# Optimization experiments

Measured on AMD Instinct MI355X. Metric: run time of the kernel, lower is better.

The kernel has to match this reference:

```python
import jax, jax.numpy as jnp
import numpy as np

N_DRUG, N_TARGET, N_EDGES, H = 50000, 20000, 500000, 256


def setup_inputs() -> dict:
    key = jax.random.key(0)
    ks = jax.random.split(key, 6)
    s = 1.0 / np.sqrt(2 * H)
    return {
        "z_drug": jax.random.normal(ks[0], (N_DRUG, H), dtype=jnp.float32),
        "z_target": jax.random.normal(ks[1], (N_TARGET, H), dtype=jnp.float32),
        "row": jax.random.randint(ks[2], (N_EDGES,), 0, N_DRUG, dtype=jnp.int64),
        "col": jax.random.randint(ks[3], (N_EDGES,), 0, N_TARGET, dtype=jnp.int64),
        "W1": jax.random.normal(ks[4], (2 * H, H), dtype=jnp.float32) * s,
        "b1": jnp.zeros((H,), dtype=jnp.float32),
        "W2": jax.random.normal(ks[5], (H, 1), dtype=jnp.float32) * (1.0 / np.sqrt(H)),
        "b2": jnp.zeros((1,), dtype=jnp.float32),
    }


def reference(z_drug, z_target, row, col, W1, b1, W2, b2):
    # gather endpoint embeddings by edge index, concat -> [E, 2H]
    zc = jnp.concatenate([z_drug[row], z_target[col]], axis=-1)
    h = jax.nn.relu(zc @ W1 + b1)          # [E, H]
    return h @ W2 + b2                     # [E, 1]
```

## Files before the change

kernel.cpp:

```cpp
#include <hip/hip_runtime.h>
#include <hip/hip_bf16.h>
#include <stdint.h>


typedef unsigned short u16;
typedef __attribute__((ext_vector_type(8))) short short8;
typedef __attribute__((ext_vector_type(4))) float f32x4;

#define HDIM 256
#define KDIM 512
#define BK 64

__device__ __forceinline__ u16 f2bf(float f) {
  union { float f; uint32_t u; } v; v.f = f;
  uint32_t u = v.u;
  return (u16)((u + 0x7fffu + ((u >> 16) & 1u)) >> 16);
}
__device__ __forceinline__ u16 f2h(float f) {
  union { _Float16 h; u16 u; } v; v.h = (_Float16)f;
  return v.u;
}
__device__ __forceinline__ float h2f(u16 b) {
  union { _Float16 h; u16 u; } v; v.u = b;
  return (float)v.h;
}

__device__ __forceinline__ void gl2lds16(const void* g, void* l) {
  __builtin_amdgcn_global_load_lds(
      (const __attribute__((address_space(1))) unsigned int*)g,
      (__attribute__((address_space(3))) unsigned int*)l,
      16, 0, 0);
}

__global__ void prep_w1t(const float* __restrict__ w1, u16* __restrict__ w1t) {
  const int b = blockIdx.x;
  __shared__ float tile[64][65];
  const int k0 = (b >> 2) * 64, n0 = (b & 3) * 64;
  const int tx = threadIdx.x & 63, ty = threadIdx.x >> 6;
#pragma unroll
  for (int i = ty; i < 64; i += 4)
    tile[i][tx] = w1[(size_t)(k0 + i) * HDIM + n0 + tx];
  __syncthreads();
#pragma unroll
  for (int i = ty; i < 64; i += 4)
    w1t[(size_t)(n0 + i) * KDIM + k0 + tx] = f2bf(tile[tx][i]);
}

__global__ __launch_bounds__(256, 2) void uv_gemm(
    const float* __restrict__ zdf, const float* __restrict__ ztf,
    const u16* __restrict__ w1t, const float* __restrict__ b1,
    u16* __restrict__ Uh, u16* __restrict__ Vh,
    int ND, int NT, int nUb) {
  __shared__ u16 lB[2][128 * BK];

  const int bid = blockIdx.x;
  const int isV = (bid >= nUb);
  const int lb  = isV ? (bid - nUb) : bid;
  const float* zf = isV ? ztf : zdf;
  u16* Oh = isV ? Vh : Uh;
  const int NR = isV ? NT : ND;
  const int r0 = (lb >> 1) * 128;
  const int n0 = (lb & 1) * 128;
  const int kb = isV ? 4 : 0;

  const int tid   = threadIdx.x;
  const int wid   = tid >> 6;
  const int lane  = tid & 63;
  const int r8    = lane >> 3;
  const int slog  = ((lane & 7) ^ (r8 & 7)) * 8;
  const int colid = lane & 15;
  const int quad  = lane >> 4;
  const int csw   = colid & 7;

  const u16* pB = w1t + (uint32_t)(n0 + wid * 32 + r8) * KDIM + slog;
  u16* lBw0 = &lB[0][(wid * 32) * BK];
  u16* lBw1 = &lB[1][(wid * 32) * BK];

  uint32_t offR[2];
#pragma unroll
  for (int rt = 0; rt < 2; ++rt) {
    int r = min(r0 + wid * 32 + rt * 16 + colid, NR - 1);
    offR[rt] = (uint32_t)r * HDIM;
  }

  f32x4 acc[2][8];
#pragma unroll
  for (int i = 0; i < 2; ++i)
#pragma unroll
    for (int j = 0; j < 8; ++j) acc[i][j] = f32x4{0.f, 0.f, 0.f, 0.f};

  float4 a32[2][2][2][2];
  short8 aB[2][2][2];

  auto loadA = [&](int kc, int buf) {
#pragma unroll
    for (int rt = 0; rt < 2; ++rt)
#pragma unroll
      for (int s = 0; s < 2; ++s) {
        const float* p = zf + offR[rt] + kc * BK + s * 32 + quad * 8;
        a32[buf][rt][s][0] = ((const float4*)p)[0];
        a32[buf][rt][s][1] = ((const float4*)p)[1];
      }
  };
  auto cvtA = [&](int buf) {
#pragma unroll
    for (int rt = 0; rt < 2; ++rt)
#pragma unroll
      for (int s = 0; s < 2; ++s) {
        float4 lo = a32[buf][rt][s][0], hi = a32[buf][rt][s][1];
        short8 r;
        r[0] = (short)f2bf(lo.x); r[1] = (short)f2bf(lo.y);
        r[2] = (short)f2bf(lo.z); r[3] = (short)f2bf(lo.w);
        r[4] = (short)f2bf(hi.x); r[5] = (short)f2bf(hi.y);
        r[6] = (short)f2bf(hi.z); r[7] = (short)f2bf(hi.w);
        aB[buf][rt][s] = r;
      }
  };
  auto stageB = [&](int kch, u16* dst) {
#pragma unroll
    for (int t = 0; t < 4; ++t)
      gl2lds16(pB + (size_t)t * 8 * KDIM + kch * BK, dst + t * 8 * BK);
  };

  stageB(kb, lBw0);
  loadA(0, 0);
  asm volatile("s_waitcnt vmcnt(0)" ::: "memory");
  cvtA(0);
  __builtin_amdgcn_s_barrier();

#pragma unroll
  for (int kc = 0; kc < 4; ++kc) {
    const int cur = kc & 1, nxt = cur ^ 1;
    if (kc < 3) {
      stageB(kb + kc + 1, nxt ? lBw1 : lBw0);
      loadA(kc + 1, nxt);
    }
#pragma unroll
    for (int s = 0; s < 2; ++s) {
      const int sl = s * 4 + quad;
      __builtin_amdgcn_s_setprio(1);
#pragma unroll
      for (int ct = 0; ct < 8; ++ct) {
        short8 bF = *(const short8*)
            &lB[cur][(ct * 16 + colid) * BK + ((sl ^ csw) * 8)];
        acc[0][ct] = __builtin_amdgcn_mfma_f32_16x16x32_bf16(
            aB[cur][0][s], bF, acc[0][ct], 0, 0, 0);
        acc[1][ct] = __builtin_amdgcn_mfma_f32_16x16x32_bf16(
            aB[cur][1][s], bF, acc[1][ct], 0, 0, 0);
      }
      __builtin_amdgcn_s_setprio(0);
    }
    if (kc < 3) {
      asm volatile("s_waitcnt vmcnt(0)" ::: "memory");
      cvtA(nxt);
      __builtin_amdgcn_s_barrier();
    }
  }

  float b1v[8];
#pragma unroll
  for (int ct = 0; ct < 8; ++ct)
    b1v[ct] = isV ? 0.f : b1[n0 + ct * 16 + colid];
#pragma unroll
  for (int rt = 0; rt < 2; ++rt)
#pragma unroll
    for (int j = 0; j < 4; ++j) {
      int r = r0 + wid * 32 + rt * 16 + quad * 4 + j;
      if (r < NR) {
#pragma unroll
        for (int ct = 0; ct < 8; ++ct)
          Oh[(size_t)r * HDIM + n0 + ct * 16 + colid] =
              f2h(acc[rt][ct][j] + b1v[ct]);
      }
    }
}

__global__ __launch_bounds__(256, 8) void edge_kernel(
    const u16* __restrict__ U, const u16* __restrict__ V,
    const int* __restrict__ row, const int* __restrict__ col,
    const float* __restrict__ w2, const float* __restrict__ b2,
    float* __restrict__ out, int E) {
  const int tid  = threadIdx.x;
  const int lane = tid & 63;
  const int wid  = tid >> 6;
  const int li   = lane & 7;
  const int eg   = lane >> 3;

  float w2v[32];
#pragma unroll
  for (int i = 0; i < 32; ++i) w2v[i] = w2[li * 32 + i];
  const float b2v = b2[0];

  for (int base = blockIdx.x * 32; base < E; base += gridDim.x * 32) {
    const int e  = base + wid * 8 + eg;
    const int ee = min(e, E - 1);
    const short8* up = (const short8*)(U + (size_t)row[ee] * HDIM + li * 32);
    const short8* vp = (const short8*)(V + (size_t)col[ee] * HDIM + li * 32);
    short8 ub[4], vb[4];
#pragma unroll
    for (int t = 0; t < 4; ++t) { ub[t] = up[t]; vb[t] = vp[t]; }
    float s = 0.f;
#pragma unroll
    for (int t = 0; t < 4; ++t)
#pragma unroll
      for (int i = 0; i < 8; ++i) {
        float h = h2f((u16)ub[t][i]) + h2f((u16)vb[t][i]);
        s += fmaxf(h, 0.f) * w2v[t * 8 + i];
      }
    s += __shfl_xor(s, 1, 8);
    s += __shfl_xor(s, 2, 8);
    s += __shfl_xor(s, 4, 8);
    if (li == 0 && e < E) out[e] = s + b2v;
  }
}

__global__ void fallback_kernel(
    const float* __restrict__ zd, const float* __restrict__ zt,
    const int* __restrict__ row, const int* __restrict__ col,
    const float* __restrict__ W1, const float* __restrict__ b1,
    const float* __restrict__ W2, const float* __restrict__ b2,
    float* __restrict__ out, int E) {
  __shared__ float zc[16][512];
  __shared__ float red[4][16];
  const int e0 = blockIdx.x * 16;
  const int tid = threadIdx.x;
  for (int i = tid; i < 16 * 512; i += 256) {
    int e = i >> 9, k = i & 511;
    int ge = min(e0 + e, E - 1);
    zc[e][k] = (k < HDIM) ? zd[(size_t)row[ge] * HDIM + k]
                          : zt[(size_t)col[ge] * HDIM + (k - HDIM)];
  }
  __syncthreads();
  float acc[16];
#pragma unroll
  for (int e = 0; e < 16; ++e) acc[e] = 0.f;
  for (int k = 0; k < KDIM; ++k) {
    float w = W1[k * HDIM + tid];
#pragma unroll
    for (int e = 0; e < 16; ++e) acc[e] += zc[e][k] * w;
  }
  float wv = W2[tid], bv = b1[tid];
  const int lane = tid & 63, wid = tid >> 6;
#pragma unroll
  for (int e = 0; e < 16; ++e) {
    float pv = fmaxf(acc[e] + bv, 0.f) * wv;
#pragma unroll
    for (int off = 32; off >= 1; off >>= 1) pv += __shfl_down(pv, off, 64);
    if (lane == 0) red[wid][e] = pv;
  }
  __syncthreads();
  if (tid < 16) {
    int ge = e0 + tid;
    if (ge < E)
      out[ge] = red[0][tid] + red[1][tid] + red[2][tid] + red[3][tid] + b2[0];
  }
}

extern "C" void kernel_launch(void* const* d_in, const int* in_sizes, int n_in,
                              void* d_out, int out_size, void* d_ws, size_t ws_size,
                              hipStream_t stream) {
  const float* zd_f = (const float*)d_in[0];
  const float* zt_f = (const float*)d_in[1];
  const int*   row  = (const int*)d_in[2];
  const int*   col  = (const int*)d_in[3];
  const float* W1   = (const float*)d_in[4];
  const float* b1   = (const float*)d_in[5];
  const float* W2   = (const float*)d_in[6];
  const float* b2   = (const float*)d_in[7];
  float* out = (float*)d_out;

  const int E  = in_sizes[2];
  const int ND = in_sizes[0] / HDIM;
  const int NT = in_sizes[1] / HDIM;

  size_t off_w1t = 0;
  size_t off_U   = (size_t)KDIM * HDIM * sizeof(u16);
  size_t off_V   = off_U + (size_t)ND * HDIM * sizeof(u16);
  size_t need    = off_V + (size_t)NT * HDIM * sizeof(u16);

  if (ws_size >= need) {
    u16* w1t = (u16*)((char*)d_ws + off_w1t);
    u16* Uh  = (u16*)((char*)d_ws + off_U);
    u16* Vh  = (u16*)((char*)d_ws + off_V);
    const int nUb = ((ND + 127) / 128) * 2;
    const int nVb = ((NT + 127) / 128) * 2;
    prep_w1t<<<32, 256, 0, stream>>>(W1, w1t);
    uv_gemm<<<nUb + nVb, 256, 0, stream>>>(zd_f, zt_f, w1t, b1, Uh, Vh,
                                           ND, NT, nUb);
    int egrid = (E + 31) / 32;
    if (egrid > 2048) egrid = 2048;
    edge_kernel<<<egrid, 256, 0, stream>>>(Uh, Vh, row, col, W2, b2,
                                           out, E);
  } else {
    fallback_kernel<<<(E + 15) / 16, 256, 0, stream>>>(
        zd_f, zt_f, row, col, W1, b1, W2, b2, out, E);
  }
}
```

Before: 267.4 us.

## Bucket-sort edges by drug row and widen uv_gemm tiles to full H

Adds a histogram, scan and scatter pass that bins edges by row index in groups of 16, so the edge kernel gathers U rows in a roughly sorted order and gets better cache locality. The uv_gemm now computes all 256 output columns per block instead of two 128-column halves, which halves the number of A-matrix reads from fp32 inputs at the cost of more accumulator registers and a larger LDS tile. The sort adds several small kernel launches and atomics over 500k edges, and the output writes now land in scattered order.

```diff
diff --git a/kernel.cpp b/kernel.cpp
--- a/kernel.cpp
+++ b/kernel.cpp
@@ -10,6 +10,7 @@
 #define HDIM 256
 #define KDIM 512
 #define BK 64
+#define BIN_SHIFT 4
 
 __device__ __forceinline__ u16 f2bf(float f) {
   union { float f; uint32_t u; } v; v.f = f;
@@ -46,12 +47,53 @@
     w1t[(size_t)(n0 + i) * KDIM + k0 + tx] = f2bf(tile[tx][i]);
 }
 
+__global__ void hist_kernel(const int* __restrict__ row, int* __restrict__ bins,
+                            int E, int NB) {
+  __shared__ int lh[4096];
+  for (int i = threadIdx.x; i < NB; i += 256) lh[i] = 0;
+  __syncthreads();
+  for (int e = blockIdx.x * 256 + threadIdx.x; e < E; e += gridDim.x * 256)
+    atomicAdd(&lh[row[e] >> BIN_SHIFT], 1);
+  __syncthreads();
+  for (int i = threadIdx.x; i < NB; i += 256) {
+    int c = lh[i];
+    if (c) atomicAdd(&bins[i], c);
+  }
+}
+
+__global__ void scan_kernel(int* __restrict__ bins, int NB) {
+  __shared__ int part[256];
+  const int t = threadIdx.x;
+  const int per = (NB + 255) / 256;
+  const int lo = t * per, hi = min(lo + per, NB);
+  int s = 0;
+  for (int i = lo; i < hi; ++i) s += bins[i];
+  part[t] = s;
+  __syncthreads();
+  if (t == 0) {
+    int a = 0;
+    for (int i = 0; i < 256; ++i) { int c = part[i]; part[i] = a; a += c; }
+  }
+  __syncthreads();
+  int run = part[t];
+  for (int i = lo; i < hi; ++i) { int c = bins[i]; bins[i] = run; run += c; }
+}
+
+__global__ void scatter_kernel(const int* __restrict__ row,
+                               int* __restrict__ cursor,
+                               int* __restrict__ perm, int E) {
+  for (int e = blockIdx.x * 256 + threadIdx.x; e < E; e += gridDim.x * 256) {
+    int pos = atomicAdd(&cursor[row[e] >> BIN_SHIFT], 1);
+    perm[pos] = e;
+  }
+}
+
 __global__ __launch_bounds__(256, 2) void uv_gemm(
     const float* __restrict__ zdf, const float* __restrict__ ztf,
     const u16* __restrict__ w1t, const float* __restrict__ b1,
     u16* __restrict__ Uh, u16* __restrict__ Vh,
     int ND, int NT, int nUb) {
-  __shared__ u16 lB[2][128 * BK];
+  __shared__ u16 lB[2][HDIM * BK];
 
   const int bid = blockIdx.x;
   const int isV = (bid >= nUb);
@@ -59,8 +101,7 @@
   const float* zf = isV ? ztf : zdf;
   u16* Oh = isV ? Vh : Uh;
   const int NR = isV ? NT : ND;
-  const int r0 = (lb >> 1) * 128;
-  const int n0 = (lb & 1) * 128;
+  const int r0 = lb * 128;
   const int kb = isV ? 4 : 0;
 
   const int tid   = threadIdx.x;
@@ -72,9 +113,9 @@
   const int quad  = lane >> 4;
   const int csw   = colid & 7;
 
-  const u16* pB = w1t + (uint32_t)(n0 + wid * 32 + r8) * KDIM + slog;
-  u16* lBw0 = &lB[0][(wid * 32) * BK];
-  u16* lBw1 = &lB[1][(wid * 32) * BK];
+  const u16* pB = w1t + (uint32_t)(wid * 64 + r8) * KDIM + slog;
+  u16* lBw0 = &lB[0][(wid * 64) * BK];
+  u16* lBw1 = &lB[1][(wid * 64) * BK];
 
   uint32_t offR[2];
 #pragma unroll
@@ -83,23 +124,23 @@
     offR[rt] = (uint32_t)r * HDIM;
   }
 
-  f32x4 acc[2][8];
+  f32x4 acc[2][16];
 #pragma unroll
   for (int i = 0; i < 2; ++i)
 #pragma unroll
-    for (int j = 0; j < 8; ++j) acc[i][j] = f32x4{0.f, 0.f, 0.f, 0.f};
-
-  float4 a32[2][2][2][2];
+    for (int j = 0; j < 16; ++j) acc[i][j] = f32x4{0.f, 0.f, 0.f, 0.f};
+
+  float4 a32[2][2][2];
   short8 aB[2][2][2];
 
-  auto loadA = [&](int kc, int buf) {
+  auto loadA = [&](int kc) {
 #pragma unroll
     for (int rt = 0; rt < 2; ++rt)
 #pragma unroll
       for (int s = 0; s < 2; ++s) {
         const float* p = zf + offR[rt] + kc * BK + s * 32 + quad * 8;
-        a32[buf][rt][s][0] = ((const float4*)p)[0];
-        a32[buf][rt][s][1] = ((const float4*)p)[1];
+        a32[rt][s][0] = ((const float4*)p)[0];
+        a32[rt][s][1] = ((const float4*)p)[1];
       }
   };
   auto cvtA = [&](int buf) {
@@ -107,7 +148,7 @@
     for (int rt = 0; rt < 2; ++rt)
 #pragma unroll
       for (int s = 0; s < 2; ++s) {
-        float4 lo = a32[buf][rt][s][0], hi = a32[buf][rt][s][1];
+        float4 lo = a32[rt][s][0], hi = a32[rt][s][1];
         short8 r;
         r[0] = (short)f2bf(lo.x); r[1] = (short)f2bf(lo.y);
         r[2] = (short)f2bf(lo.z); r[3] = (short)f2bf(lo.w);
@@ -118,12 +159,12 @@
   };
   auto stageB = [&](int kch, u16* dst) {
 #pragma unroll
-    for (int t = 0; t < 4; ++t)
+    for (int t = 0; t < 8; ++t)
       gl2lds16(pB + (size_t)t * 8 * KDIM + kch * BK, dst + t * 8 * BK);
   };
 
+  loadA(0);
   stageB(kb, lBw0);
-  loadA(0, 0);
   asm volatile("s_waitcnt vmcnt(0)" ::: "memory");
   cvtA(0);
   __builtin_amdgcn_s_barrier();
@@ -132,15 +173,15 @@
   for (int kc = 0; kc < 4; ++kc) {
     const int cur = kc & 1, nxt = cur ^ 1;
     if (kc < 3) {
+      loadA(kc + 1);
       stageB(kb + kc + 1, nxt ? lBw1 : lBw0);
-      loadA(kc + 1, nxt);
     }
 #pragma unroll
     for (int s = 0; s < 2; ++s) {
       const int sl = s * 4 + quad;
       __builtin_amdgcn_s_setprio(1);
 #pragma unroll
-      for (int ct = 0; ct < 8; ++ct) {
+      for (int ct = 0; ct < 16; ++ct) {
         short8 bF = *(const short8*)
             &lB[cur][(ct * 16 + colid) * BK + ((sl ^ csw) * 8)];
         acc[0][ct] = __builtin_amdgcn_mfma_f32_16x16x32_bf16(
@@ -157,10 +198,10 @@
     }
   }
 
-  float b1v[8];
-#pragma unroll
-  for (int ct = 0; ct < 8; ++ct)
-    b1v[ct] = isV ? 0.f : b1[n0 + ct * 16 + colid];
+  float b1v[16];
+#pragma unroll
+  for (int ct = 0; ct < 16; ++ct)
+    b1v[ct] = isV ? 0.f : b1[ct * 16 + colid];
 #pragma unroll
   for (int rt = 0; rt < 2; ++rt)
 #pragma unroll
@@ -168,11 +209,52 @@
       int r = r0 + wid * 32 + rt * 16 + quad * 4 + j;
       if (r < NR) {
 #pragma unroll
-        for (int ct = 0; ct < 8; ++ct)
-          Oh[(size_t)r * HDIM + n0 + ct * 16 + colid] =
+        for (int ct = 0; ct < 16; ++ct)
+          Oh[(size_t)r * HDIM + ct * 16 + colid] =
               f2h(acc[rt][ct][j] + b1v[ct]);
       }
     }
+}
+
+__global__ __launch_bounds__(256, 8) void edge_kernel_sorted(
+    const u16* __restrict__ U, const u16* __restrict__ V,
+    const int* __restrict__ perm,
+    const int* __restrict__ row, const int* __restrict__ col,
+    const float* __restrict__ w2, const float* __restrict__ b2,
+    float* __restrict__ out, int E) {
+  const int tid  = threadIdx.x;
+  const int lane = tid & 63;
+  const int wid  = tid >> 6;
+  const int li   = lane & 7;
+  const int eg   = lane >> 3;
+
+  float w2v[32];
+#pragma unroll
+  for (int i = 0; i < 32; ++i) w2v[i] = w2[li * 32 + i];
+  const float b2v = b2[0];
+
+  for (int base = blockIdx.x * 32; base < E; base += gridDim.x * 32) {
+    const int idx = base + wid * 8 + eg;
+    const int ii  = min(idx, E - 1);
+    const int pe  = perm[ii];
+    const short8* up = (const short8*)(U + (size_t)row[pe] * HDIM + li * 32);
+    const short8* vp = (const short8*)(V + (size_t)col[pe] * HDIM + li * 32);
+    short8 ub[4], vb[4];
+#pragma unroll
+    for (int t = 0; t < 4; ++t) { ub[t] = up[t]; vb[t] = vp[t]; }
+    float s = 0.f;
+#pragma unroll
+    for (int t = 0; t < 4; ++t)
+#pragma unroll
+      for (int i = 0; i < 8; ++i) {
+        float h = h2f((u16)ub[t][i]) + h2f((u16)vb[t][i]);
+        s += fmaxf(h, 0.f) * w2v[t * 8 + i];
+      }
+    s += __shfl_xor(s, 1, 8);
+    s += __shfl_xor(s, 2, 8);
+    s += __shfl_xor(s, 4, 8);
+    if (li == 0 && idx < E) out[pe] = s + b2v;
+  }
 }
 
 __global__ __launch_bounds__(256, 8) void edge_kernel(
@@ -185,12 +267,10 @@
   const int wid  = tid >> 6;
   const int li   = lane & 7;
   const int eg   = lane >> 3;
-
   float w2v[32];
 #pragma unroll
   for (int i = 0; i < 32; ++i) w2v[i] = w2[li * 32 + i];
   const float b2v = b2[0];
-
   for (int base = blockIdx.x * 32; base < E; base += gridDim.x * 32) {
     const int e  = base + wid * 8 + eg;
     const int ee = min(e, E - 1);
@@ -272,25 +352,41 @@
   const int E  = in_sizes[2];
   const int ND = in_sizes[0] / HDIM;
   const int NT = in_sizes[1] / HDIM;
-
-  size_t off_w1t = 0;
-  size_t off_U   = (size_t)KDIM * HDIM * sizeof(u16);
-  size_t off_V   = off_U + (size_t)ND * HDIM * sizeof(u16);
-  size_t need    = off_V + (size_t)NT * HDIM * sizeof(u16);
-
-  if (ws_size >= need) {
+  const int NB = (ND + (1 << BIN_SHIFT) - 1) >> BIN_SHIFT;
+
+  size_t off_w1t  = 0;
+  size_t off_U    = (size_t)KDIM * HDIM * sizeof(u16);
+  size_t off_V    = off_U + (size_t)ND * HDIM * sizeof(u16);
+  size_t off_bins = off_V + (size_t)NT * HDIM * sizeof(u16);
+  size_t off_perm = off_bins + 16384;
+  size_t need_sorted = off_perm + (size_t)E * sizeof(int);
+  size_t need_plain  = off_bins;
+
+  if (ws_size >= need_plain) {
     u16* w1t = (u16*)((char*)d_ws + off_w1t);
     u16* Uh  = (u16*)((char*)d_ws + off_U);
     u16* Vh  = (u16*)((char*)d_ws + off_V);
-    const int nUb = ((ND + 127) / 128) * 2;
-    const int nVb = ((NT + 127) / 128) * 2;
+    const int nUb = (ND + 127) / 128;
+    const int nVb = (NT + 127) / 128;
     prep_w1t<<<32, 256, 0, stream>>>(W1, w1t);
     uv_gemm<<<nUb + nVb, 256, 0, stream>>>(zd_f, zt_f, w1t, b1, Uh, Vh,
                                            ND, NT, nUb);
     int egrid = (E + 31) / 32;
     if (egrid > 2048) egrid = 2048;
-    edge_kernel<<<egrid, 256, 0, stream>>>(Uh, Vh, row, col, W2, b2,
-                                           out, E);
+
+    if (ws_size >= need_sorted && NB <= 4096) {
+      int* bins = (int*)((char*)d_ws + off_bins);
+      int* perm = (int*)((char*)d_ws + off_perm);
+      hipMemsetAsync(bins, 0, (size_t)NB * sizeof(int), stream);
+      hist_kernel<<<256, 256, 0, stream>>>(row, bins, E, NB);
+      scan_kernel<<<1, 256, 0, stream>>>(bins, NB);
+      scatter_kernel<<<256, 256, 0, stream>>>(row, bins, perm, E);
+      edge_kernel_sorted<<<egrid, 256, 0, stream>>>(Uh, Vh, perm, row, col,
+                                                    W2, b2, out, E);
+    } else {
+      edge_kernel<<<egrid, 256, 0, stream>>>(Uh, Vh, row, col, W2, b2,
+                                             out, E);
+    }
   } else {
     fallback_kernel<<<(E + 15) / 16, 256, 0, stream>>>(
         zd_f, zt_f, row, col, W1, b1, W2, b2, out, E);
```

Measured after the change: 301.3 us. +12.7%, slower.

## Bin-sort edges by drug row and swizzle edge blocks across XCDs

Applied to the files above, without the earlier changes.

Adds a counting sort of edges by row bin: a histogram step fused into the W1 transpose kernel, a single-block scan and an atomic scatter that writes packed (row, col, edge id) records. A new edge kernel walks the sorted records, with block IDs remapped so that neighbouring row bins land on the same XCD. The aim is more L2 reuse of the U-row gathers. The cost is two extra launches, a global atomic scatter and an extra 16-byte-per-edge permutation buffer.

```diff
diff --git a/kernel.cpp b/kernel.cpp
--- a/kernel.cpp
+++ b/kernel.cpp
@@ -10,6 +10,8 @@
 #define HDIM 256
 #define KDIM 512
 #define BK 64
+#define BIN_SHIFT 4
+#define NHIST 64
 
 __device__ __forceinline__ u16 f2bf(float f) {
   union { float f; uint32_t u; } v; v.f = f;
@@ -32,18 +34,68 @@
       16, 0, 0);
 }
 
-__global__ void prep_w1t(const float* __restrict__ w1, u16* __restrict__ w1t) {
+__global__ void prep_hist(const float* __restrict__ w1, u16* __restrict__ w1t,
+                          const int* __restrict__ row, int* __restrict__ bins2d,
+                          int E, int NB) {
   const int b = blockIdx.x;
   __shared__ float tile[64][65];
-  const int k0 = (b >> 2) * 64, n0 = (b & 3) * 64;
-  const int tx = threadIdx.x & 63, ty = threadIdx.x >> 6;
-#pragma unroll
-  for (int i = ty; i < 64; i += 4)
-    tile[i][tx] = w1[(size_t)(k0 + i) * HDIM + n0 + tx];
+  __shared__ int lh[3200];
+  if (b < 32) {
+    const int k0 = (b >> 2) * 64, n0 = (b & 3) * 64;
+    const int tx = threadIdx.x & 63, ty = threadIdx.x >> 6;
+#pragma unroll
+    for (int i = ty; i < 64; i += 4)
+      tile[i][tx] = w1[(size_t)(k0 + i) * HDIM + n0 + tx];
+    __syncthreads();
+#pragma unroll
+    for (int i = ty; i < 64; i += 4)
+      w1t[(size_t)(n0 + i) * KDIM + k0 + tx] = f2bf(tile[tx][i]);
+  } else {
+    const int hb = b - 32;
+    for (int i = threadIdx.x; i < NB; i += 256) lh[i] = 0;
+    __syncthreads();
+    for (int e = hb * 256 + threadIdx.x; e < E; e += NHIST * 256)
+      atomicAdd(&lh[row[e] >> BIN_SHIFT], 1);
+    __syncthreads();
+    for (int i = threadIdx.x; i < NB; i += 256)
+      bins2d[(size_t)hb * NB + i] = lh[i];
+  }
+}
+
+__global__ void scan_kernel(const int* __restrict__ bins2d,
+                            int* __restrict__ cursor, int NB) {
+  __shared__ int part[256];
+  const int t = threadIdx.x;
+  const int per = (NB + 255) / 256;
+  const int lo = t * per, hi = min(lo + per, NB);
+  int s = 0;
+  for (int i = lo; i < hi; ++i) {
+    int tot = 0;
+#pragma unroll 4
+    for (int b = 0; b < NHIST; ++b) tot += bins2d[(size_t)b * NB + i];
+    cursor[i] = tot;
+    s += tot;
+  }
+  part[t] = s;
   __syncthreads();
-#pragma unroll
-  for (int i = ty; i < 64; i += 4)
-    w1t[(size_t)(n0 + i) * KDIM + k0 + tx] = f2bf(tile[tx][i]);
+  if (t == 0) {
+    int a = 0;
+    for (int i = 0; i < 256; ++i) { int c = part[i]; part[i] = a; a += c; }
+  }
+  __syncthreads();
+  int run = part[t];
+  for (int i = lo; i < hi; ++i) { int c = cursor[i]; cursor[i] = run; run += c; }
+}
+
+__global__ void scatter_kernel(const int* __restrict__ row,
+                               const int* __restrict__ col,
+                               int* __restrict__ cursor,
+                               int4* __restrict__ perm4, int E) {
+  for (int e = blockIdx.x * 256 + threadIdx.x; e < E; e += gridDim.x * 256) {
+    int r = row[e];
+    int pos = atomicAdd(&cursor[r >> BIN_SHIFT], 1);
+    perm4[pos] = make_int4(r, col[e], e, 0);
+  }
 }
 
 __global__ __launch_bounds__(256, 2) void uv_gemm(
@@ -173,6 +225,53 @@
               f2h(acc[rt][ct][j] + b1v[ct]);
       }
     }
+}
+
+__global__ __launch_bounds__(256, 8) void edge_kernel_sorted(
+    const u16* __restrict__ U, const u16* __restrict__ V,
+    const int4* __restrict__ perm4,
+    const float* __restrict__ w2, const float* __restrict__ b2,
+    float* __restrict__ out, int E) {
+  const int tid  = threadIdx.x;
+  const int lane = tid & 63;
+  const int wid  = tid >> 6;
+  const int li   = lane & 7;
+  const int eg   = lane >> 3;
+
+  float w2v[32];
+#pragma unroll
+  for (int i = 0; i < 32; ++i) w2v[i] = w2[li * 32 + i];
+  const float b2v = b2[0];
+
+  const int nwg = gridDim.x;
+  const int q = nwg >> 3, r = nwg & 7;
+  const int xcd = blockIdx.x & 7, sub = blockIdx.x >> 3;
+  const int swz = (xcd < r ? xcd * (q + 1) : r * (q + 1) + (xcd - r) * q) + sub;
+  const int base0 = swz * 256;
+
+#pragma unroll
+  for (int it = 0; it < 8; ++it) {
+    const int idx = base0 + it * 32 + wid * 8 + eg;
+    const int ii  = min(idx, E - 1);
+    const int4 rc = perm4[ii];
+    const short8* up = (const short8*)(U + (size_t)rc.x * HDIM + li * 32);
+    const short8* vp = (const short8*)(V + (size_t)rc.y * HDIM + li * 32);
+    short8 ub[4], vb[4];
+#pragma unroll
+    for (int t = 0; t < 4; ++t) { ub[t] = up[t]; vb[t] = vp[t]; }
+    float s = 0.f;
+#pragma unroll
+    for (int t = 0; t < 4; ++t)
+#pragma unroll
+      for (int i = 0; i < 8; ++i) {
+        float h = h2f((u16)ub[t][i]) + h2f((u16)vb[t][i]);
+        s += fmaxf(h, 0.f) * w2v[t * 8 + i];
+      }
+    s += __shfl_xor(s, 1, 8);
+    s += __shfl_xor(s, 2, 8);
+    s += __shfl_xor(s, 4, 8);
+    if (li == 0 && idx < E) out[rc.z] = s + b2v;
+  }
 }
 
 __global__ __launch_bounds__(256, 8) void edge_kernel(
@@ -185,12 +284,10 @@
   const int wid  = tid >> 6;
   const int li   = lane & 7;
   const int eg   = lane >> 3;
-
   float w2v[32];
 #pragma unroll
   for (int i = 0; i < 32; ++i) w2v[i] = w2[li * 32 + i];
   const float b2v = b2[0];
-
   for (int base = blockIdx.x * 32; base < E; base += gridDim.x * 32) {
     const int e  = base + wid * 8 + eg;
     const int ee = min(e, E - 1);
@@ -256,6 +353,8 @@
   }
 }
 
+static inline size_t align256(size_t x) { return (x + 255) & ~(size_t)255; }
+
 extern "C" void kernel_launch(void* const* d_in, const int* in_sizes, int n_in,
                               void* d_out, int out_size, void* d_ws, size_t ws_size,
                               hipStream_t stream) {
@@ -272,25 +371,45 @@
   const int E  = in_sizes[2];
   const int ND = in_sizes[0] / HDIM;
   const int NT = in_sizes[1] / HDIM;
+  const int NB = (ND + (1 << BIN_SHIFT) - 1) >> BIN_SHIFT;
 
   size_t off_w1t = 0;
-  size_t off_U   = (size_t)KDIM * HDIM * sizeof(u16);
-  size_t off_V   = off_U + (size_t)ND * HDIM * sizeof(u16);
-  size_t need    = off_V + (size_t)NT * HDIM * sizeof(u16);
-
-  if (ws_size >= need) {
+  size_t off_U   = align256((size_t)KDIM * HDIM * sizeof(u16));
+  size_t off_V   = align256(off_U + (size_t)ND * HDIM * sizeof(u16));
+  size_t off_b2d = align256(off_V + (size_t)NT * HDIM * sizeof(u16));
+  size_t off_cur = align256(off_b2d + (size_t)NHIST * NB * sizeof(int));
+  size_t off_pm  = align256(off_cur + (size_t)NB * sizeof(int));
+  size_t need_sorted = off_pm + (size_t)E * sizeof(int4);
+  size_t need_plain  = off_b2d;
+
+  if (ws_size >= need_plain) {
     u16* w1t = (u16*)((char*)d_ws + off_w1t);
     u16* Uh  = (u16*)((char*)d_ws + off_U);
     u16* Vh  = (u16*)((char*)d_ws + off_V);
     const int nUb = ((ND + 127) / 128) * 2;
     const int nVb = ((NT + 127) / 128) * 2;
-    prep_w1t<<<32, 256, 0, stream>>>(W1, w1t);
-    uv_gemm<<<nUb + nVb, 256, 0, stream>>>(zd_f, zt_f, w1t, b1, Uh, Vh,
-                                           ND, NT, nUb);
-    int egrid = (E + 31) / 32;
-    if (egrid > 2048) egrid = 2048;
-    edge_kernel<<<egrid, 256, 0, stream>>>(Uh, Vh, row, col, W2, b2,
-                                           out, E);
+
+    if (ws_size >= need_sorted && NB <= 3200) {
+      int*  bins2d = (int*)((char*)d_ws + off_b2d);
+      int*  cursor = (int*)((char*)d_ws + off_cur);
+      int4* perm4  = (int4*)((char*)d_ws + off_pm);
+      prep_hist<<<32 + NHIST, 256, 0, stream>>>(W1, w1t, row, bins2d, E, NB);
+      scan_kernel<<<1, 256, 0, stream>>>(bins2d, cursor, NB);
+      scatter_kernel<<<256, 256, 0, stream>>>(row, col, cursor, perm4, E);
+      uv_gemm<<<nUb + nVb, 256, 0, stream>>>(zd_f, zt_f, w1t, b1, Uh, Vh,
+                                             ND, NT, nUb);
+      const int nwg = (E + 255) / 256;
+      edge_kernel_sorted<<<nwg, 256, 0, stream>>>(Uh, Vh, perm4, W2, b2,
+                                                  out, E);
+    } else {
+      prep_hist<<<32, 256, 0, stream>>>(W1, w1t, row, (int*)nullptr, 0, NB);
+      uv_gemm<<<nUb + nVb, 256, 0, stream>>>(zd_f, zt_f, w1t, b1, Uh, Vh,
+                                             ND, NT, nUb);
+      int egrid = (E + 31) / 32;
+      if (egrid > 2048) egrid = 2048;
+      edge_kernel<<<egrid, 256, 0, stream>>>(Uh, Vh, row, col, W2, b2,
+                                             out, E);
+    }
   } else {
     fallback_kernel<<<(E + 15) / 16, 256, 0, stream>>>(
         zd_f, zt_f, row, col, W1, b1, W2, b2, out, E);
```

Result: slower. 328.7 us (+22.9%).
